# Kernel tuning notes

Measured on AMD Instinct MI355X. Metric: run time of the kernel, lower is better.

## Reference

```python
import jax, jax.numpy as jnp
import numpy as np

N = 100000
E = 1600000
F_IN = 64
F_OUT = 64
K = 3


def setup_inputs() -> dict:
    key = jax.random.key(0)
    k1, k2, k3, k4, k5 = jax.random.split(key, 5)
    x = jax.random.normal(k1, (N, F_IN), dtype=jnp.float32)
    rows = jnp.sort(jax.random.randint(k2, (E,), 0, N, dtype=jnp.int32))
    cols = jax.random.randint(k3, (E,), 0, N, dtype=jnp.int32)
    vals = jax.random.uniform(k4, (E,), dtype=jnp.float32)
    # xavier-uniform-ish weights
    limit = float(np.sqrt(6.0 / (F_IN + F_OUT)))
    weight = jax.random.uniform(k5, (K, F_IN, F_OUT), dtype=jnp.float32,
                                minval=-limit, maxval=limit)
    bias = jnp.zeros((F_OUT,), dtype=jnp.float32)
    return {"x": x, "rows": rows, "cols": cols, "vals": vals,
            "weight": weight, "bias": bias}


def _spmm(vals, rows, cols, h):
    # adj @ h with adj in COO form: out[i] = sum_{e: rows[e]==i} vals[e] * h[cols[e]]
    return jax.ops.segment_sum(vals[:, None] * h[cols], rows, num_segments=N)


def reference(x, rows, cols, vals, weight, bias):
    Tx_0 = x                              # T_0(L) x = x
    Tx_1 = _spmm(vals, rows, cols, x)     # T_1(L) x = L x
    out = Tx_0 @ weight[0] + Tx_1 @ weight[1]
    for k in range(2, K):                 # Chebyshev recurrence (K is small/static)
        Tx_2 = 2.0 * _spmm(vals, rows, cols, Tx_1) - Tx_0
        out = out + Tx_2 @ weight[k]
        Tx_0, Tx_1 = Tx_1, Tx_2
    return out + bias
```

## Files before the change

### kernel.cpp

```cpp
#include <hip/hip_runtime.h>

constexpr int NN = 100000;
constexpr int NE = 1600000;
constexpr int F  = 64;

typedef short bf16x8 __attribute__((ext_vector_type(8)));
typedef float f32x4  __attribute__((ext_vector_type(4)));

__device__ __forceinline__ float bf_lo(unsigned u) { return __uint_as_float(u << 16); }
__device__ __forceinline__ float bf_hi(unsigned u) { return __uint_as_float(u & 0xFFFF0000u); }
__device__ __forceinline__ unsigned pack_bf16(float a, float b) {
    unsigned ua = __float_as_uint(a);
    unsigned ub = __float_as_uint(b);
    ua = (ua + 0x7FFFu + ((ua >> 16) & 1u)) >> 16;
    ub = (ub + 0x7FFFu + ((ub >> 16) & 1u)) & 0xFFFF0000u;
    return ua | ub;
}

constexpr int B_CVT = NN * F / 8 / 256;
constexpr int B_RP  = NE / 256;
constexpr int B_W   = 192 * 64 / 256;

__global__ __launch_bounds__(256)
void prep_k(const float* __restrict__ x, ushort* __restrict__ xb,
            const int* __restrict__ rows, int* __restrict__ row_ptr,
            const float* __restrict__ w, ushort* __restrict__ wt) {
    const int b = blockIdx.x;
    if (b < B_CVT) {
        int tid = b * 256 + threadIdx.x;
        const float4* p = (const float4*)x + (size_t)tid * 2;
        float4 a = p[0], c = p[1];
        uint4 o = make_uint4(pack_bf16(a.x, a.y), pack_bf16(a.z, a.w),
                             pack_bf16(c.x, c.y), pack_bf16(c.z, c.w));
        ((uint4*)xb)[tid] = o;
    } else if (b < B_CVT + B_RP) {
        int e = (b - B_CVT) * 256 + threadIdx.x;
        int r1 = rows[e];
        int r2 = (e == NE - 1) ? NN : rows[e + 1];
        for (int r = r1 + 1; r <= r2; ++r) row_ptr[r] = e + 1;
        if (e == 0)
            for (int r = 0; r <= r1; ++r) row_ptr[r] = 0;
    } else {
        int tid = (b - B_CVT - B_RP) * 256 + threadIdx.x;
        int k = tid >> 6, n = tid & 63;
        unsigned u = __float_as_uint(w[tid]);
        u = (u + 0x7FFFu + ((u >> 16) & 1u)) >> 16;
        wt[n * 192 + k] = (ushort)u;
    }
}

template<bool SECOND>
__global__ __launch_bounds__(256)
void spmm_k(const int* __restrict__ row_ptr, const int* __restrict__ cols,
            const float* __restrict__ vals, const ushort* __restrict__ src,
            const ushort* __restrict__ x0, ushort* __restrict__ dst) {
    const int lane = threadIdx.x & 63;
    const int fgrp = lane & 7;
    const int g    = lane >> 3;
    const int r    = (blockIdx.x * 4 + (threadIdx.x >> 6)) * 8 + g;
    const int e0 = row_ptr[r];
    const int e1 = row_ptr[r + 1];
    const int deg = e1 - e0;
    int maxdeg = deg;
    maxdeg = max(maxdeg, __shfl_xor(maxdeg, 8));
    maxdeg = max(maxdeg, __shfl_xor(maxdeg, 16));
    maxdeg = max(maxdeg, __shfl_xor(maxdeg, 32));

    float acc[8] = {};
    #pragma unroll 2
    for (int s = 0; s < maxdeg; ++s) {
        const bool act = s < deg;
        int ec = act ? (e0 + s) : (e1 - 1);
        ec = ec < 0 ? 0 : ec;
        const int   cj = cols[ec];
        const float vv = vals[ec];
        const float vj = act ? vv : 0.f;
        uint4 raw = *(const uint4*)(src + (size_t)cj * F + fgrp * 8);
        acc[0] += vj * bf_lo(raw.x); acc[1] += vj * bf_hi(raw.x);
        acc[2] += vj * bf_lo(raw.y); acc[3] += vj * bf_hi(raw.y);
        acc[4] += vj * bf_lo(raw.z); acc[5] += vj * bf_hi(raw.z);
        acc[6] += vj * bf_lo(raw.w); acc[7] += vj * bf_hi(raw.w);
    }

    float o[8];
    if (SECOND) {
        uint4 xr = *(const uint4*)(x0 + (size_t)r * F + fgrp * 8);
        o[0] = 2.f * acc[0] - bf_lo(xr.x); o[1] = 2.f * acc[1] - bf_hi(xr.x);
        o[2] = 2.f * acc[2] - bf_lo(xr.y); o[3] = 2.f * acc[3] - bf_hi(xr.y);
        o[4] = 2.f * acc[4] - bf_lo(xr.z); o[5] = 2.f * acc[5] - bf_hi(xr.z);
        o[6] = 2.f * acc[6] - bf_lo(xr.w); o[7] = 2.f * acc[7] - bf_hi(xr.w);
    } else {
        #pragma unroll
        for (int t = 0; t < 8; ++t) o[t] = acc[t];
    }
    uint4 ov = make_uint4(pack_bf16(o[0], o[1]), pack_bf16(o[2], o[3]),
                          pack_bf16(o[4], o[5]), pack_bf16(o[6], o[7]));
    *(uint4*)(dst + (size_t)r * F + fgrp * 8) = ov;
}

__global__ __launch_bounds__(256)
void dense_k(const ushort* __restrict__ xb, const ushort* __restrict__ t1,
             const ushort* __restrict__ t2, const ushort* __restrict__ wt,
             const float* __restrict__ bias, float* __restrict__ out) {
    __shared__ float lds[4][16 * 68];
    const int tid  = threadIdx.x;
    const int lane = tid & 63;
    const int wv   = tid >> 6;
    const int row0 = blockIdx.x * 64 + wv * 16;
    const int m    = lane & 15;
    const int quad = lane >> 4;
    int arow = row0 + m;
    if (arow >= NN) arow = NN - 1;

    f32x4 acc[4] = {};
    #pragma unroll
    for (int kb = 0; kb < 6; ++kb) {
        const int kbase = kb * 32;
        const ushort* seg = (kb < 2) ? xb : (kb < 4) ? t1 : t2;
        const int off = (kbase & 63) + quad * 8;
        bf16x8 a = *(const bf16x8*)(seg + (size_t)arow * F + off);
        #pragma unroll
        for (int t = 0; t < 4; ++t) {
            const int n = t * 16 + m;
            bf16x8 b = *(const bf16x8*)(wt + (size_t)n * 192 + kbase + quad * 8);
            acc[t] = __builtin_amdgcn_mfma_f32_16x16x32_bf16(a, b, acc[t], 0, 0, 0);
        }
    }

    float* sl = lds[wv];
    #pragma unroll
    for (int t = 0; t < 4; ++t) {
        const float bv = bias[t * 16 + m];
        #pragma unroll
        for (int rr = 0; rr < 4; ++rr)
            sl[(quad * 4 + rr) * 68 + t * 16 + m] = acc[t][rr] + bv;
    }
    __syncthreads();
    const int m4 = (lane & 15) * 4;
    #pragma unroll
    for (int p = 0; p < 4; ++p) {
        const int rl = p * 4 + (lane >> 4);
        const int grow = row0 + rl;
        f32x4 v = *(const f32x4*)(sl + rl * 68 + m4);
        if (grow < NN)
            *(f32x4*)(out + (size_t)grow * F + m4) = v;
    }
}

extern "C" void kernel_launch(void* const* d_in, const int* in_sizes, int n_in,
                              void* d_out, int out_size, void* d_ws, size_t ws_size,
                              hipStream_t stream) {
    const float* x    = (const float*)d_in[0];
    const int*   rows = (const int*)  d_in[1];
    const int*   cols = (const int*)  d_in[2];
    const float* vals = (const float*)d_in[3];
    const float* w    = (const float*)d_in[4];
    const float* bias = (const float*)d_in[5];
    float* out = (float*)d_out;

    char* ws = (char*)d_ws;
    int* row_ptr = (int*)ws;
    size_t off = (((size_t)(NN + 1) * sizeof(int)) + 255) & ~(size_t)255;
    ushort* xb  = (ushort*)(ws + off);
    ushort* t1b = xb  + (size_t)NN * F;
    ushort* t2b = t1b + (size_t)NN * F;
    ushort* wt  = t2b + (size_t)NN * F;

    prep_k<<<B_CVT + B_RP + B_W, 256, 0, stream>>>(x, xb, rows, row_ptr, w, wt);
    spmm_k<false><<<NN / 32, 256, 0, stream>>>(row_ptr, cols, vals, xb,  nullptr, t1b);
    spmm_k<true ><<<NN / 32, 256, 0, stream>>>(row_ptr, cols, vals, t1b, xb,      t2b);
    dense_k<<<(NN + 63) / 64, 256, 0, stream>>>(xb, t1b, t2b, wt, bias, out);
}
```

Before: 186.1 us.

## Fuse second SpMM into dense MFMA kernel and interleave col/val edges

The second Chebyshev SpMM is fused into the dense MFMA kernel, and its T2 rows are staged in LDS instead of round-tripping a full bf16 buffer through global memory. This removes one kernel launch and the T2 write plus re-read. The prep kernel also packs cols and vals into an int2 edge array, so each gather issues one 8-byte load instead of two separate loads. The cost is an extra 12.8MB write in prep, and the fused kernel has more LDS use and a sync, which may lower occupancy for the latency-bound gather.

```diff
diff --git a/kernel.cpp b/kernel.cpp
--- a/kernel.cpp
+++ b/kernel.cpp
@@ -23,8 +23,10 @@
 
 __global__ __launch_bounds__(256)
 void prep_k(const float* __restrict__ x, ushort* __restrict__ xb,
-            const int* __restrict__ rows, int* __restrict__ row_ptr,
-            const float* __restrict__ w, ushort* __restrict__ wt) {
+            const int* __restrict__ rows, const int* __restrict__ cols,
+            const float* __restrict__ vals, int* __restrict__ row_ptr,
+            int2* __restrict__ ev, const float* __restrict__ w,
+            ushort* __restrict__ wt) {
     const int b = blockIdx.x;
     if (b < B_CVT) {
         int tid = b * 256 + threadIdx.x;
@@ -36,6 +38,7 @@
     } else if (b < B_CVT + B_RP) {
         int e = (b - B_CVT) * 256 + threadIdx.x;
         int r1 = rows[e];
+        ev[e] = make_int2(cols[e], __float_as_int(vals[e]));
         int r2 = (e == NE - 1) ? NN : rows[e + 1];
         for (int r = r1 + 1; r <= r2; ++r) row_ptr[r] = e + 1;
         if (e == 0)
@@ -49,11 +52,9 @@
     }
 }
 
-template<bool SECOND>
 __global__ __launch_bounds__(256)
-void spmm_k(const int* __restrict__ row_ptr, const int* __restrict__ cols,
-            const float* __restrict__ vals, const ushort* __restrict__ src,
-            const ushort* __restrict__ x0, ushort* __restrict__ dst) {
+void spmm1_k(const int* __restrict__ row_ptr, const int2* __restrict__ ev,
+             const ushort* __restrict__ src, ushort* __restrict__ dst) {
     const int lane = threadIdx.x & 63;
     const int fgrp = lane & 7;
     const int g    = lane >> 3;
@@ -72,53 +73,88 @@
         const bool act = s < deg;
         int ec = act ? (e0 + s) : (e1 - 1);
         ec = ec < 0 ? 0 : ec;
-        const int   cj = cols[ec];
-        const float vv = vals[ec];
-        const float vj = act ? vv : 0.f;
-        uint4 raw = *(const uint4*)(src + (size_t)cj * F + fgrp * 8);
+        const int2 em = ev[ec];
+        const float vj = act ? __int_as_float(em.y) : 0.f;
+        uint4 raw = *(const uint4*)(src + (size_t)em.x * F + fgrp * 8);
         acc[0] += vj * bf_lo(raw.x); acc[1] += vj * bf_hi(raw.x);
         acc[2] += vj * bf_lo(raw.y); acc[3] += vj * bf_hi(raw.y);
         acc[4] += vj * bf_lo(raw.z); acc[5] += vj * bf_hi(raw.z);
         acc[6] += vj * bf_lo(raw.w); acc[7] += vj * bf_hi(raw.w);
     }
-
-    float o[8];
-    if (SECOND) {
-        uint4 xr = *(const uint4*)(x0 + (size_t)r * F + fgrp * 8);
+    uint4 ov = make_uint4(pack_bf16(acc[0], acc[1]), pack_bf16(acc[2], acc[3]),
+                          pack_bf16(acc[4], acc[5]), pack_bf16(acc[6], acc[7]));
+    *(uint4*)(dst + (size_t)r * F + fgrp * 8) = ov;
+}
+
+__global__ __launch_bounds__(256)
+void fused_k(const int* __restrict__ row_ptr, const int2* __restrict__ ev,
+             const ushort* __restrict__ xb, const ushort* __restrict__ t1b,
+             const ushort* __restrict__ wt, const float* __restrict__ bias,
+             float* __restrict__ out) {
+    __shared__ ushort t2s[64 * 72];
+    __shared__ float slab[4][16 * 68];
+    const int tid  = threadIdx.x;
+    const int lane = tid & 63;
+    const int wv   = tid >> 6;
+    const int fgrp = lane & 7;
+    const int g    = lane >> 3;
+
+    #pragma unroll
+    for (int u = 0; u < 2; ++u) {
+        const int row_local = wv * 16 + u * 8 + g;
+        const int r  = blockIdx.x * 64 + row_local;
+        const int rc = min(r, NN - 1);
+        const int e0 = row_ptr[rc];
+        const int e1 = (r < NN) ? row_ptr[rc + 1] : e0;
+        const int deg = e1 - e0;
+        int maxdeg = deg;
+        maxdeg = max(maxdeg, __shfl_xor(maxdeg, 8));
+        maxdeg = max(maxdeg, __shfl_xor(maxdeg, 16));
+        maxdeg = max(maxdeg, __shfl_xor(maxdeg, 32));
+
+        float acc[8] = {};
+        #pragma unroll 2
+        for (int s = 0; s < maxdeg; ++s) {
+            const bool act = s < deg;
+            int ec = act ? (e0 + s) : (e1 - 1);
+            ec = ec < 0 ? 0 : ec;
+            const int2 em = ev[ec];
+            const float vj = act ? __int_as_float(em.y) : 0.f;
+            uint4 raw = *(const uint4*)(t1b + (size_t)em.x * F + fgrp * 8);
+            acc[0] += vj * bf_lo(raw.x); acc[1] += vj * bf_hi(raw.x);
+            acc[2] += vj * bf_lo(raw.y); acc[3] += vj * bf_hi(raw.y);
+            acc[4] += vj * bf_lo(raw.z); acc[5] += vj * bf_hi(raw.z);
+            acc[6] += vj * bf_lo(raw.w); acc[7] += vj * bf_hi(raw.w);
+        }
+        uint4 xr = *(const uint4*)(xb + (size_t)rc * F + fgrp * 8);
+        float o[8];
         o[0] = 2.f * acc[0] - bf_lo(xr.x); o[1] = 2.f * acc[1] - bf_hi(xr.x);
         o[2] = 2.f * acc[2] - bf_lo(xr.y); o[3] = 2.f * acc[3] - bf_hi(xr.y);
         o[4] = 2.f * acc[4] - bf_lo(xr.z); o[5] = 2.f * acc[5] - bf_hi(xr.z);
         o[6] = 2.f * acc[6] - bf_lo(xr.w); o[7] = 2.f * acc[7] - bf_hi(xr.w);
-    } else {
-        #pragma unroll
-        for (int t = 0; t < 8; ++t) o[t] = acc[t];
-    }
-    uint4 ov = make_uint4(pack_bf16(o[0], o[1]), pack_bf16(o[2], o[3]),
-                          pack_bf16(o[4], o[5]), pack_bf16(o[6], o[7]));
-    *(uint4*)(dst + (size_t)r * F + fgrp * 8) = ov;
-}
-
-__global__ __launch_bounds__(256)
-void dense_k(const ushort* __restrict__ xb, const ushort* __restrict__ t1,
-             const ushort* __restrict__ t2, const ushort* __restrict__ wt,
-             const float* __restrict__ bias, float* __restrict__ out) {
-    __shared__ float lds[4][16 * 68];
-    const int tid  = threadIdx.x;
-    const int lane = tid & 63;
-    const int wv   = tid >> 6;
+        uint4 ov = make_uint4(pack_bf16(o[0], o[1]), pack_bf16(o[2], o[3]),
+                              pack_bf16(o[4], o[5]), pack_bf16(o[6], o[7]));
+        *(uint4*)(t2s + row_local * 72 + fgrp * 8) = ov;
+    }
+    __syncthreads();
+
     const int row0 = blockIdx.x * 64 + wv * 16;
     const int m    = lane & 15;
     const int quad = lane >> 4;
-    int arow = row0 + m;
-    if (arow >= NN) arow = NN - 1;
+    const int arow = min(row0 + m, NN - 1);
 
     f32x4 acc[4] = {};
     #pragma unroll
     for (int kb = 0; kb < 6; ++kb) {
         const int kbase = kb * 32;
-        const ushort* seg = (kb < 2) ? xb : (kb < 4) ? t1 : t2;
         const int off = (kbase & 63) + quad * 8;
-        bf16x8 a = *(const bf16x8*)(seg + (size_t)arow * F + off);
+        bf16x8 a;
+        if (kb < 4) {
+            const ushort* seg = (kb < 2) ? xb : t1b;
+            a = *(const bf16x8*)(seg + (size_t)arow * F + off);
+        } else {
+            a = *(const bf16x8*)(t2s + (wv * 16 + m) * 72 + off);
+        }
         #pragma unroll
         for (int t = 0; t < 4; ++t) {
             const int n = t * 16 + m;
@@ -127,7 +163,7 @@
         }
     }
 
-    float* sl = lds[wv];
+    float* sl = slab[wv];
     #pragma unroll
     for (int t = 0; t < 4; ++t) {
         const float bv = bias[t * 16 + m];
@@ -163,11 +199,12 @@
     size_t off = (((size_t)(NN + 1) * sizeof(int)) + 255) & ~(size_t)255;
     ushort* xb  = (ushort*)(ws + off);
     ushort* t1b = xb  + (size_t)NN * F;
-    ushort* t2b = t1b + (size_t)NN * F;
-    ushort* wt  = t2b + (size_t)NN * F;
-
-    prep_k<<<B_CVT + B_RP + B_W, 256, 0, stream>>>(x, xb, rows, row_ptr, w, wt);
-    spmm_k<false><<<NN / 32, 256, 0, stream>>>(row_ptr, cols, vals, xb,  nullptr, t1b);
-    spmm_k<true ><<<NN / 32, 256, 0, stream>>>(row_ptr, cols, vals, t1b, xb,      t2b);
-    dense_k<<<(NN + 63) / 64, 256, 0, stream>>>(xb, t1b, t2b, wt, bias, out);
-}
+    ushort* wt  = t1b + (size_t)NN * F;
+    int2*   ev  = (int2*)(wt + 192 * 64);
+
+    prep_k<<<B_CVT + B_RP + B_W, 256, 0, stream>>>(x, xb, rows, cols, vals,
+                                                   row_ptr, ev, w, wt);
+    spmm1_k<<<NN / 32, 256, 0, stream>>>(row_ptr, ev, xb, t1b);
+    fused_k<<<(NN + 63) / 64, 256, 0, stream>>>(row_ptr, ev, xb, t1b, wt,
+                                                bias, out);
+}
```

Measured after the change: 208.1 us. 11.8% more time.
